# Performance work log

Measured on AMD Instinct MI355X. Metric: run time of the kernel, lower is better.

## Reference

```python
import jax, jax.numpy as jnp
import numpy as np

B, S, D_IN, D_OUT, H = 4, 2048, 2048, 2048, 16
HD = D_OUT // H  # head_dim = 128


def setup_inputs() -> dict:
    key = jax.random.key(0)
    ks = jax.random.split(key, 5)
    s = 0.02
    return {
        "x": jax.random.normal(ks[0], (B, S, D_IN), dtype=jnp.float32),
        "W_q": jax.random.normal(ks[1], (D_IN, D_OUT), dtype=jnp.float32) * s,
        "W_k": jax.random.normal(ks[2], (D_IN, D_OUT), dtype=jnp.float32) * s,
        "W_v": jax.random.normal(ks[3], (D_IN, D_OUT), dtype=jnp.float32) * s,
        "W_o": jax.random.normal(ks[4], (D_OUT, D_OUT), dtype=jnp.float32) * s,
        "b_o": jnp.zeros((D_OUT,), dtype=jnp.float32),
    }


def reference(x, W_q, W_k, W_v, W_o, b_o):
    b, n, _ = x.shape
    # projections (qkv_bias=False), split into heads: [b, h, n, hd]
    q = (x @ W_q).reshape(b, n, H, HD).transpose(0, 2, 1, 3)
    k = (x @ W_k).reshape(b, n, H, HD).transpose(0, 2, 1, 3)
    v = (x @ W_v).reshape(b, n, H, HD).transpose(0, 2, 1, 3)
    # scores [b, h, n, n], causal mask (triu, diagonal=1) applied BEFORE scaling
    scores = jnp.einsum("bhqd,bhkd->bhqk", q, k)
    causal = jnp.triu(jnp.ones((n, n), dtype=bool), k=1)
    scores = jnp.where(causal, -jnp.inf, scores)
    scale = jnp.asarray(HD, scores.dtype) ** 0.5
    attn = jax.nn.softmax(scores / scale, axis=-1)
    ctx = jnp.einsum("bhqk,bhkd->bhqd", attn, v)
    ctx = ctx.transpose(0, 2, 1, 3).reshape(b, n, D_OUT)
    return ctx @ W_o + b_o
```

## Files before the change

### kernel.cpp

```cpp
#include <hip/hip_runtime.h>
#include <hip/hip_bf16.h>
#include <math.h>

#define H_   16
#define S_   2048
#define D_   2048
#define HD_  128
#define B_   4
#define M_   8192

typedef __attribute__((ext_vector_type(8))) short short8;
typedef __attribute__((ext_vector_type(4))) short short4v;
typedef __attribute__((ext_vector_type(4))) float f32x4;

__device__ __forceinline__ short f2bf(float f) {
  unsigned u = __float_as_uint(f);
  u += 0x7fff + ((u >> 16) & 1);
  return (short)(u >> 16);
}

__device__ __forceinline__ unsigned pk2(float a, float b) {
  __hip_bfloat162 h = __float22bfloat162_rn(float2{a, b});
  union { __hip_bfloat162 h2; unsigned u; } c;
  c.h2 = h;
  return c.u;
}

__device__ __forceinline__ void async16(const void* g, void* l) {
  __builtin_amdgcn_global_load_lds(
      (const __attribute__((address_space(1))) void*)g,
      (__attribute__((address_space(3))) void*)l, 16, 0, 0);
}

__global__ void k_cvtx(const float* __restrict__ x, short* __restrict__ o, int n4) {
  const int i = blockIdx.x * 256 + threadIdx.x;
  if (i >= n4) return;
  const float4 f = ((const float4*)x)[i];
  short4v s;
  s.x = f2bf(f.x); s.y = f2bf(f.y); s.z = f2bf(f.z); s.w = f2bf(f.w);
  ((short4v*)o)[i] = s;
}

__global__ void k_wtrans(const float* __restrict__ W, short* __restrict__ Wt) {
  __shared__ float t[32][33];
  const int n0 = blockIdx.x << 5, k0 = blockIdx.y << 5;
  const int tc = threadIdx.x & 31, tr = threadIdx.x >> 5;
#pragma unroll
  for (int i = 0; i < 32; i += 8)
    t[tr + i][tc] = W[(size_t)(k0 + tr + i) * D_ + n0 + tc];
  __syncthreads();
#pragma unroll
  for (int i = 0; i < 32; i += 8)
    Wt[(size_t)(n0 + tr + i) * D_ + k0 + tc] = f2bf(t[tc][tr + i]);
}


#define GBAR() asm volatile("s_barrier" ::: "memory")
#define WLG0()                                          \
  do {                                                  \
    asm volatile("s_waitcnt lgkmcnt(0)" ::: "memory");  \
    __builtin_amdgcn_sched_barrier(0);                  \
  } while (0)

#define STG_A(b, mh, t)                                           \
  do {                                                            \
    const size_t o_ = (size_t)(t) * 64 + (size_t)(mh) * 64 * K;   \
    async16(Ag0 + o_, &As[b][mh][ldst]);                          \
    async16(Ag1 + o_, &As[b][mh][4096 + ldst]);                   \
  } while (0)

#define STG_B(b, nh, t)                                           \
  do {                                                            \
    const size_t o_ = (size_t)(t) * 64 + (size_t)(nh) * 32 * K;   \
    async16(Bg0 + o_, &Bs[b][nh][ldst]);                          \
    async16(Bg1 + o_, &Bs[b][nh][4096 + ldst]);                   \
  } while (0)

#define LDS_A(b, mh)                                                     \
  do {                                                                   \
    const char* a_ = (const char*)&As[b][mh][0];                         \
    _Pragma("unroll") for (int mi_ = 0; mi_ < 4; ++mi_) {                \
      af[mi_ * 2]     = *(const short8*)(a_ + rdA + mi_ * 2048 + cc0);   \
      af[mi_ * 2 + 1] = *(const short8*)(a_ + rdA + mi_ * 2048 + cc1);   \
    }                                                                    \
  } while (0)

#define LDS_B(b, nh, BF)                                                 \
  do {                                                                   \
    const char* b_ = (const char*)&Bs[b][nh][0];                         \
    _Pragma("unroll") for (int ni_ = 0; ni_ < 2; ++ni_) {                \
      BF[ni_ * 2]     = *(const short8*)(b_ + rdB + ni_ * 2048 + cc0);   \
      BF[ni_ * 2 + 1] = *(const short8*)(b_ + rdB + ni_ * 2048 + cc1);   \
    }                                                                    \
  } while (0)

#define QUAD(mh, nh, BF)                                                   \
  do {                                                                     \
    __builtin_amdgcn_s_setprio(1);                                         \
    _Pragma("unroll") for (int mi_ = 0; mi_ < 4; ++mi_)                    \
    _Pragma("unroll") for (int ni_ = 0; ni_ < 2; ++ni_) {                  \
      acc[(mh) * 4 + mi_][(nh) * 2 + ni_] =                                \
          __builtin_amdgcn_mfma_f32_16x16x32_bf16(                         \
              af[mi_ * 2], BF[ni_ * 2],                                    \
              acc[(mh) * 4 + mi_][(nh) * 2 + ni_], 0, 0, 0);               \
      acc[(mh) * 4 + mi_][(nh) * 2 + ni_] =                                \
          __builtin_amdgcn_mfma_f32_16x16x32_bf16(                         \
              af[mi_ * 2 + 1], BF[ni_ * 2 + 1],                            \
              acc[(mh) * 4 + mi_][(nh) * 2 + ni_], 0, 0, 0);               \
    }                                                                      \
    __builtin_amdgcn_s_setprio(0);                                         \
  } while (0)

#define TILE(T, b)                                                  \
  do {                                                              \
                           \
    LDS_A(b, 0);                                                    \
    LDS_B(b, 0, bf0);                                               \
    if ((T) + 1 < NT) STG_A((b) ^ 1, 1, (T) + 1);                   \
    asm volatile("s_waitcnt lgkmcnt(8)" ::: "memory");              \
    GBAR();                                                         \
    WLG0();                                                         \
    QUAD(0, 0, bf0);                                                \
    GBAR();                                                         \
                           \
    LDS_B(b, 1, bf1);                                               \
    if ((T) + 2 < NT) STG_A(b, 0, (T) + 2);                         \
    GBAR();                                                         \
    WLG0();                                                         \
    QUAD(0, 1, bf1);                                                \
    GBAR();                                                         \
                           \
    LDS_A(b, 1);                                                    \
    if ((T) + 2 < NT) STG_B(b, 0, (T) + 2);                         \
    GBAR();                                                         \
    WLG0();                                                         \
    QUAD(1, 0, bf0);                                                \
    GBAR();                                                         \
                           \
    if ((T) + 2 < NT) STG_B(b, 1, (T) + 2);                         \
    if ((T) + 2 < NT)                                               \
      asm volatile("s_waitcnt vmcnt(6)" ::: "memory");              \
    else if ((T) + 1 < NT)                                          \
      asm volatile("s_waitcnt vmcnt(0)" ::: "memory");              \
    GBAR();                                                         \
    QUAD(1, 1, bf1);                                                \
    GBAR();                                                         \
  } while (0)

template <int MODE>
__global__ __launch_bounds__(512, 2)
void k_gemm256(const short* __restrict__ A, const short* __restrict__ Bt,
               void* __restrict__ C0, void* __restrict__ C1, void* __restrict__ C2,
               const float* __restrict__ bias, int M, int N, int K) {
  __shared__ __align__(16) short As[2][2][8192];
  __shared__ __align__(16) short Bs[2][2][8192];
  const int tid = threadIdx.x;
  const int lane = tid & 63;
  const int wave = tid >> 6;
  const int ln = lane & 15, lq = lane >> 4;
  const int wr = wave >> 2, wc = wave & 3;
  const int bn = blockIdx.x << 8;
  const int bm = blockIdx.y << 8;
  const int NT = K >> 6;

  const int r0 = wave * 8 + (lane >> 3);
  const int k0 = ((lane & 7) ^ ((lane >> 3) & 7)) << 3;
  const short* Ag0 = A  + (size_t)(bm + r0) * K + k0;
  const short* Ag1 = A  + (size_t)(bm + 128 + r0) * K + k0;
  const short* Bg0 = Bt + (size_t)(bn + ((r0 >> 5) << 6) + (r0 & 31)) * K + k0;
  const short* Bg1 = Bt + (size_t)(bn + (((r0 >> 5) + 2) << 6) + (r0 & 31)) * K + k0;
  const int ldst = wave * 512;

  const int swz = (ln & 7) << 4;
  const int rdA = (wr * 64 + ln) * 128;
  const int rdB = (wc * 32 + ln) * 128;
  const int cc0 = (lq * 16) ^ swz;
  const int cc1 = (64 + lq * 16) ^ swz;

  f32x4 acc[8][4];
#pragma unroll
  for (int i = 0; i < 8; i++)
#pragma unroll
    for (int j = 0; j < 4; j++) acc[i][j] = (f32x4)0.0f;

  STG_A(0, 0, 0);
  STG_B(0, 0, 0);
  STG_B(0, 1, 0);
  STG_A(0, 1, 0);
  asm volatile("s_waitcnt vmcnt(4)" ::: "memory");
  STG_A(1, 0, 1);
  STG_B(1, 0, 1);
  STG_B(1, 1, 1);
  asm volatile("s_waitcnt vmcnt(6)" ::: "memory");
  GBAR();

  short8 af[8];
  short8 bf0[4], bf1[4];

#pragma unroll 1
  for (int T = 0; T < NT; T += 2) {
    TILE(T, 0);
    TILE(T + 1, 1);
  }

  if (MODE == 0) {
    const int proj = bn >> 11;
    const int cb = bn & 2047;
    if (proj < 2) {
      short* C = (short*)(proj == 0 ? C0 : C1);
#pragma unroll
      for (int mi = 0; mi < 8; mi++)
#pragma unroll
        for (int ni = 0; ni < 4; ni++) {
          const int col = cb + wc * 64 + ni * 16 + ln;
          const int h = col >> 7, d = col & 127;
#pragma unroll
          for (int r = 0; r < 4; r++) {
            const int row = bm + wr * 128 + mi * 16 + lq * 4 + r;
            const int bb = row >> 11, s = row & 2047;
            C[((size_t)((bb * H_ + h) * S_ + s)) * HD_ + d] = f2bf(acc[mi][ni][r]);
          }
        }
    } else {
      short* C = (short*)C2;
#pragma unroll
      for (int mi = 0; mi < 8; mi++)
#pragma unroll
        for (int ni = 0; ni < 4; ni++) {
          const int col = cb + wc * 64 + ni * 16 + ln;
          const int h = col >> 7, d = col & 127;
          const int row0 = bm + wr * 128 + mi * 16 + lq * 4;
          const int bb = row0 >> 11, s = row0 & 2047;
          short4v pk;
#pragma unroll
          for (int r = 0; r < 4; r++) pk[r] = f2bf(acc[mi][ni][r]);
          *(short4v*)(C + ((size_t)((bb * H_ + h) * HD_ + d)) * S_ + s) = pk;
        }
    }
  } else {
    float* C = (float*)C0;
#pragma unroll
    for (int mi = 0; mi < 8; mi++)
#pragma unroll
      for (int ni = 0; ni < 4; ni++) {
        const int col = bn + wc * 64 + ni * 16 + ln;
        const float bv = bias[col];
#pragma unroll
        for (int r = 0; r < 4; r++) {
          const int row = bm + wr * 128 + mi * 16 + lq * 4 + r;
          C[(size_t)row * N + col] = acc[mi][ni][r] + bv;
        }
      }
  }
}

__global__ __launch_bounds__(256)
void k_flash(const short* __restrict__ Q, const short* __restrict__ K,
             const short* __restrict__ Vt, short* __restrict__ ctx) {
  __shared__ __align__(16) short Ks[2][64 * 128];
  __shared__ __align__(16) short Vs[2][128 * 64];
  __shared__ __align__(16) short Ps[4 * 32 * 64];

  const int tid = threadIdx.x, lane = tid & 63, w = tid >> 6;
  const int ln = lane & 15, lq = lane >> 4;
  const int bh = blockIdx.x & 63;
  const int pr = blockIdx.x >> 6;
  const int b = bh >> 4, h = bh & 15;
  const short* Qp = Q  + (size_t)bh * S_ * HD_;
  const short* Kp = K  + (size_t)bh * S_ * HD_;
  const short* Vp = Vt + (size_t)bh * HD_ * S_;

  const float sc = 0.08838834764831845f * 1.4426950408889634f;
  const int lx = ln & 7;

  int koff[4], voff[4];
#pragma unroll
  for (int it = 0; it < 4; it++) {
    const int kr = w * 16 + it * 4 + (lane >> 4);
    koff[it] = kr * HD_ + (((lane & 15) ^ (kr & 7)) * 8);
    const int vr = w * 32 + it * 8 + (lane >> 3);
    voff[it] = vr * S_ + (((lane & 7) ^ (vr & 7)) * 8);
  }

#pragma unroll 1
  for (int pass = 0; pass < 2; pass++) {
    const int qb = pass ? (15 - pr) : pr;
    const int q0 = qb << 7;
    const int qw = q0 + w * 32;
    const int nkt = qb * 2 + 2;

    short8 qf[2][4];
#pragma unroll
    for (int nt = 0; nt < 2; nt++)
#pragma unroll
      for (int c = 0; c < 4; c++)
        qf[nt][c] = *(const short8*)(Qp + (size_t)(qw + nt * 16 + ln) * HD_ + c * 32 + lq * 8);

    f32x4 acc[8][2];
#pragma unroll
    for (int t = 0; t < 8; t++) { acc[t][0] = (f32x4)0.0f; acc[t][1] = (f32x4)0.0f; }
    float l_i[2] = {0.0f, 0.0f};

    __syncthreads();
#pragma unroll
    for (int it = 0; it < 4; it++) {
      async16(Kp + koff[it], &Ks[0][(w * 16 + it * 4) * 128]);
      async16(Vp + voff[it], &Vs[0][(w * 32 + it * 8) * 64]);
    }

#pragma unroll 1
    for (int kt = 0; kt < nkt; kt++) {
      const int k0 = kt << 6;
      const int cur = kt & 1;
      __syncthreads();
      if (kt + 1 < nkt) {
        const int nk0 = (kt + 1) << 6;
        const int nb = cur ^ 1;
#pragma unroll
        for (int it = 0; it < 4; it++) {
          async16(Kp + (size_t)nk0 * HD_ + koff[it], &Ks[nb][(w * 16 + it * 4) * 128]);
          async16(Vp + nk0 + voff[it],               &Vs[nb][(w * 32 + it * 8) * 64]);
        }
      }

      if (k0 <= qw + 31) {
        const short* KsC = Ks[cur];
        const short* VsC = Vs[cur];
        short* Pw = Ps + w * 32 * 64;
        const bool dg = (k0 + 63 > qw);

#pragma unroll
        for (int mt = 0; mt < 4; mt++) {
          f32x4 s0 = (f32x4)0.0f, s1 = (f32x4)0.0f;
#pragma unroll
          for (int c = 0; c < 4; c++) {
            short8 kf = *(const short8*)(KsC + (mt * 16 + ln) * 128 + (((4 * c + lq) ^ lx) * 8));
            s0 = __builtin_amdgcn_mfma_f32_16x16x32_bf16(kf, qf[0][c], s0, 0, 0, 0);
            s1 = __builtin_amdgcn_mfma_f32_16x16x32_bf16(kf, qf[1][c], s1, 0, 0, 0);
          }
          if (dg) {
#pragma unroll
            for (int r = 0; r < 4; r++) {
              const int kv = k0 + mt * 16 + lq * 4 + r;
              if (kv > qw + ln)      s0[r] = -INFINITY; else s0[r] *= sc;
              if (kv > qw + 16 + ln) s1[r] = -INFINITY; else s1[r] *= sc;
            }
          } else {
#pragma unroll
            for (int r = 0; r < 4; r++) { s0[r] *= sc; s1[r] *= sc; }
          }
#pragma unroll
          for (int r = 0; r < 4; r++) {
            s0[r] = exp2f(s0[r]); l_i[0] += s0[r];
            s1[r] = exp2f(s1[r]); l_i[1] += s1[r];
          }
          const int swc = (2 * mt + (lq >> 1)) ^ lx;
          const int po = swc * 8 + (lq & 1) * 4;
          *(uint2*)(Pw + ln * 64 + po)        = uint2{pk2(s0[0], s0[1]), pk2(s0[2], s0[3])};
          *(uint2*)(Pw + (16 + ln) * 64 + po) = uint2{pk2(s1[0], s1[1]), pk2(s1[2], s1[3])};
        }
        __asm__ volatile("s_waitcnt lgkmcnt(0)" ::: "memory");

#pragma unroll
        for (int c = 0; c < 2; c++) {
          const int swr = ((4 * c + lq) ^ lx) * 8;
          short8 pf0 = *(const short8*)(Pw + ln * 64 + swr);
          short8 pf1 = *(const short8*)(Pw + (16 + ln) * 64 + swr);
#pragma unroll
          for (int t = 0; t < 8; t++) {
            short8 vf = *(const short8*)(VsC + (t * 16 + ln) * 64 + swr);
            acc[t][0] = __builtin_amdgcn_mfma_f32_16x16x32_bf16(vf, pf0, acc[t][0], 0, 0, 0);
            acc[t][1] = __builtin_amdgcn_mfma_f32_16x16x32_bf16(vf, pf1, acc[t][1], 0, 0, 0);
          }
        }
      }
    }

#pragma unroll
    for (int o = 16; o < 64; o <<= 1) {
      l_i[0] += __shfl_xor(l_i[0], o, 64);
      l_i[1] += __shfl_xor(l_i[1], o, 64);
    }
    const float il[2] = {1.0f / l_i[0], 1.0f / l_i[1]};

#pragma unroll
    for (int t = 0; t < 8; t++)
#pragma unroll
      for (int nt = 0; nt < 2; nt++) {
        const int q = qw + nt * 16 + ln;
        const int d = t * 16 + lq * 4;
        uint2 o2 = {pk2(acc[t][nt][0] * il[nt], acc[t][nt][1] * il[nt]),
                    pk2(acc[t][nt][2] * il[nt], acc[t][nt][3] * il[nt])};
        *(uint2*)(ctx + ((size_t)(b * S_ + q)) * D_ + h * HD_ + d) = o2;
      }
  }
}

extern "C" void kernel_launch(void* const* d_in, const int* in_sizes, int n_in,
                              void* d_out, int out_size, void* d_ws, size_t ws_size,
                              hipStream_t stream) {
  const float* x  = (const float*)d_in[0];
  const float* Wq = (const float*)d_in[1];
  const float* Wk = (const float*)d_in[2];
  const float* Wv = (const float*)d_in[3];
  const float* Wo = (const float*)d_in[4];
  const float* bo = (const float*)d_in[5];
  float* out = (float*)d_out;

  char* ws = (char*)d_ws;
  const size_t SZ_X = (size_t)M_ * D_ * sizeof(short);
  const size_t SZ_W = (size_t)D_ * D_ * sizeof(short);
  short* xb  = (short*)(ws);
  short* Wqt = (short*)(ws + SZ_X);
  short* Wkt = (short*)(ws + SZ_X + SZ_W);
  short* Wvt = (short*)(ws + SZ_X + 2 * SZ_W);
  short* Wot = (short*)(ws + SZ_X + 3 * SZ_W);
  short* Qb  = (short*)(ws + SZ_X + 4 * SZ_W);
  short* Kb  = (short*)(ws + 2 * SZ_X + 4 * SZ_W);
  short* Vtb = (short*)(ws + 3 * SZ_X + 4 * SZ_W);
  short* ctx = (short*)(ws + 4 * SZ_X + 4 * SZ_W);

  k_cvtx<<<M_ * D_ / 4 / 256, 256, 0, stream>>>(x, xb, M_ * D_ / 4);
  dim3 tg(D_ / 32, D_ / 32);
  k_wtrans<<<tg, 256, 0, stream>>>(Wq, Wqt);
  k_wtrans<<<tg, 256, 0, stream>>>(Wk, Wkt);
  k_wtrans<<<tg, 256, 0, stream>>>(Wv, Wvt);
  k_wtrans<<<tg, 256, 0, stream>>>(Wo, Wot);

  dim3 gq(3 * D_ / 256, M_ / 256);
  k_gemm256<0><<<gq, 512, 0, stream>>>(xb, Wqt, Qb, Kb, Vtb, nullptr, M_, 3 * D_, D_);

  k_flash<<<8 * 64, 256, 0, stream>>>(Qb, Kb, Vtb, ctx);

  dim3 go(D_ / 256, M_ / 256);
  k_gemm256<1><<<go, 512, 0, stream>>>(ctx, Wot, out, nullptr, nullptr, bo, M_, D_, D_);
}
```

Measured before the change: 611.9 us.

## Split GEMM inner tile along K halves and restage A/B prefetch schedule

Each 64-wide K tile is now split into two 32-wide halves. Every phase loads 4 A fragments and 4 B fragments (covering both N halves) and issues 16 MFMAs, instead of quadrant-wise loads over the full K tile. The A stage for the next tile is issued earlier across two phases, and the prologue and vmcnt waits change to match. The explicit lgkmcnt waits and sched_barriers are dropped, leaving LDS-read waiting to the compiler. This halves the A fragment registers and is meant to spread LDS traffic and global prefetch more evenly across phases, at the risk of weaker LDS-read/MFMA overlap without the manual waits.

```diff
diff --git a/kernel.cpp b/kernel.cpp
--- a/kernel.cpp
+++ b/kernel.cpp
@@ -56,11 +56,6 @@
 
 
 #define GBAR() asm volatile("s_barrier" ::: "memory")
-#define WLG0()                                          \
-  do {                                                  \
-    asm volatile("s_waitcnt lgkmcnt(0)" ::: "memory");  \
-    __builtin_amdgcn_sched_barrier(0);                  \
-  } while (0)
 
 #define STG_A(b, mh, t)                                           \
   do {                                                            \
@@ -76,74 +71,64 @@
     async16(Bg1 + o_, &Bs[b][nh][4096 + ldst]);                   \
   } while (0)
 
-#define LDS_A(b, mh)                                                     \
+#define LDS_AF(b, mh, CC)                                                \
   do {                                                                   \
     const char* a_ = (const char*)&As[b][mh][0];                         \
-    _Pragma("unroll") for (int mi_ = 0; mi_ < 4; ++mi_) {                \
-      af[mi_ * 2]     = *(const short8*)(a_ + rdA + mi_ * 2048 + cc0);   \
-      af[mi_ * 2 + 1] = *(const short8*)(a_ + rdA + mi_ * 2048 + cc1);   \
-    }                                                                    \
-  } while (0)
-
-#define LDS_B(b, nh, BF)                                                 \
+    _Pragma("unroll") for (int mi_ = 0; mi_ < 4; ++mi_)                  \
+      af[mi_] = *(const short8*)(a_ + rdA + mi_ * 2048 + (CC));          \
+  } while (0)
+
+#define LDS_BF(b, CC, BF)                                                \
   do {                                                                   \
-    const char* b_ = (const char*)&Bs[b][nh][0];                         \
-    _Pragma("unroll") for (int ni_ = 0; ni_ < 2; ++ni_) {                \
-      BF[ni_ * 2]     = *(const short8*)(b_ + rdB + ni_ * 2048 + cc0);   \
-      BF[ni_ * 2 + 1] = *(const short8*)(b_ + rdB + ni_ * 2048 + cc1);   \
-    }                                                                    \
-  } while (0)
-
-#define QUAD(mh, nh, BF)                                                   \
-  do {                                                                     \
-    __builtin_amdgcn_s_setprio(1);                                         \
-    _Pragma("unroll") for (int mi_ = 0; mi_ < 4; ++mi_)                    \
-    _Pragma("unroll") for (int ni_ = 0; ni_ < 2; ++ni_) {                  \
-      acc[(mh) * 4 + mi_][(nh) * 2 + ni_] =                                \
-          __builtin_amdgcn_mfma_f32_16x16x32_bf16(                         \
-              af[mi_ * 2], BF[ni_ * 2],                                    \
-              acc[(mh) * 4 + mi_][(nh) * 2 + ni_], 0, 0, 0);               \
-      acc[(mh) * 4 + mi_][(nh) * 2 + ni_] =                                \
-          __builtin_amdgcn_mfma_f32_16x16x32_bf16(                         \
-              af[mi_ * 2 + 1], BF[ni_ * 2 + 1],                            \
-              acc[(mh) * 4 + mi_][(nh) * 2 + ni_], 0, 0, 0);               \
-    }                                                                      \
-    __builtin_amdgcn_s_setprio(0);                                         \
+    const char* b0_ = (const char*)&Bs[b][0][0];                         \
+    const char* b1_ = (const char*)&Bs[b][1][0];                         \
+    BF[0] = *(const short8*)(b0_ + rdB + (CC));                          \
+    BF[1] = *(const short8*)(b0_ + rdB + 2048 + (CC));                   \
+    BF[2] = *(const short8*)(b1_ + rdB + (CC));                          \
+    BF[3] = *(const short8*)(b1_ + rdB + 2048 + (CC));                   \
+  } while (0)
+
+#define QUADX(mh, BF)                                                     \
+  do {                                                                    \
+    __builtin_amdgcn_s_setprio(1);                                        \
+    _Pragma("unroll") for (int mi_ = 0; mi_ < 4; ++mi_)                   \
+    _Pragma("unroll") for (int ni_ = 0; ni_ < 4; ++ni_)                   \
+      acc[(mh) * 4 + mi_][ni_] = __builtin_amdgcn_mfma_f32_16x16x32_bf16( \
+          af[mi_], BF[ni_], acc[(mh) * 4 + mi_][ni_], 0, 0, 0);           \
+    __builtin_amdgcn_s_setprio(0);                                        \
   } while (0)
 
 #define TILE(T, b)                                                  \
   do {                                                              \
-                           \
-    LDS_A(b, 0);                                                    \
-    LDS_B(b, 0, bf0);                                               \
+                                      \
+    LDS_AF(b, 0, cc0);                                              \
+    LDS_BF(b, cc0, bf0);                                            \
+    if ((T) + 1 < NT) STG_A((b) ^ 1, 0, (T) + 1);                   \
+    GBAR();                                                         \
+    QUADX(0, bf0);                                                  \
+    GBAR();                                                         \
+                                      \
+    LDS_AF(b, 0, cc1);                                              \
+    LDS_BF(b, cc1, bf1);                                            \
     if ((T) + 1 < NT) STG_A((b) ^ 1, 1, (T) + 1);                   \
-    asm volatile("s_waitcnt lgkmcnt(8)" ::: "memory");              \
-    GBAR();                                                         \
-    WLG0();                                                         \
-    QUAD(0, 0, bf0);                                                \
-    GBAR();                                                         \
-                           \
-    LDS_B(b, 1, bf1);                                               \
-    if ((T) + 2 < NT) STG_A(b, 0, (T) + 2);                         \
-    GBAR();                                                         \
-    WLG0();                                                         \
-    QUAD(0, 1, bf1);                                                \
-    GBAR();                                                         \
-                           \
-    LDS_A(b, 1);                                                    \
+    GBAR();                                                         \
+    QUADX(0, bf1);                                                  \
+    GBAR();                                                         \
+                                      \
+    LDS_AF(b, 1, cc0);                                              \
     if ((T) + 2 < NT) STG_B(b, 0, (T) + 2);                         \
     GBAR();                                                         \
-    WLG0();                                                         \
-    QUAD(1, 0, bf0);                                                \
-    GBAR();                                                         \
-                           \
+    QUADX(1, bf0);                                                  \
+    GBAR();                                                         \
+                                      \
+    LDS_AF(b, 1, cc1);                                              \
     if ((T) + 2 < NT) STG_B(b, 1, (T) + 2);                         \
     if ((T) + 2 < NT)                                               \
-      asm volatile("s_waitcnt vmcnt(6)" ::: "memory");              \
+      asm volatile("s_waitcnt vmcnt(4)" ::: "memory");              \
     else if ((T) + 1 < NT)                                          \
       asm volatile("s_waitcnt vmcnt(0)" ::: "memory");              \
     GBAR();                                                         \
-    QUAD(1, 1, bf1);                                                \
+    QUADX(1, bf1);                                                  \
     GBAR();                                                         \
   } while (0)
 
@@ -184,17 +169,15 @@
     for (int j = 0; j < 4; j++) acc[i][j] = (f32x4)0.0f;
 
   STG_A(0, 0, 0);
+  STG_A(0, 1, 0);
   STG_B(0, 0, 0);
   STG_B(0, 1, 0);
-  STG_A(0, 1, 0);
-  asm volatile("s_waitcnt vmcnt(4)" ::: "memory");
-  STG_A(1, 0, 1);
   STG_B(1, 0, 1);
   STG_B(1, 1, 1);
-  asm volatile("s_waitcnt vmcnt(6)" ::: "memory");
+  asm volatile("s_waitcnt vmcnt(4)" ::: "memory");
   GBAR();
 
-  short8 af[8];
+  short8 af[4];
   short8 bf0[4], bf1[4];
 
 #pragma unroll 1
```

Measured after the change: 630.2 us. 3.0% more time.
